# Kernel optimization log

Measured on AMD Instinct MI355X. Metric: run time of the kernel, lower is better.

## Reference

```python
import jax, jax.numpy as jnp
import numpy as np

N_TAGS = 64
SOS, EOS, PAD = 61, 62, 63
NEG = -1000000.0
B, S = 512, 1024


def setup_inputs() -> dict:
    key = jax.random.key(0)
    k1, k2, k3 = jax.random.split(key, 3)
    emissions = jax.random.normal(k1, (B, S, N_TAGS), dtype=jnp.float32)
    tags = jax.random.randint(k2, (B, S), 0, SOS)  # real tags only
    mask = jnp.ones((B, S), dtype=jnp.float32)
    t = jax.random.uniform(k3, (N_TAGS, N_TAGS), minval=-0.1, maxval=0.1, dtype=jnp.float32)
    t = t.at[:, SOS].set(NEG)
    t = t.at[EOS, :].set(NEG)
    t = t.at[PAD, :].set(NEG)
    t = t.at[:, PAD].set(NEG)
    t = t.at[PAD, EOS].set(0.0)
    t = t.at[PAD, PAD].set(0.0)
    return {"emissions": emissions, "tags": tags, "mask": mask, "transitions": t}


def _crf_nll(emissions, tags, mask, transitions):
    b, s, _ = emissions.shape
    # ---- gold path score (vectorized over seq) ----
    first_tags = tags[:, 0]
    last_idx = mask.astype(jnp.int32).sum(1) - 1  # [B]
    last_tags = tags[jnp.arange(b), last_idx]
    e_all = jnp.take_along_axis(emissions, tags[..., None], axis=-1)[..., 0]  # [B,S]
    t_all = transitions[tags[:, :-1], tags[:, 1:]]  # [B,S-1]
    m_tail = mask[:, 1:]
    scores = (
        transitions[SOS, first_tags]
        + e_all[:, 0]
        + jnp.sum((e_all[:, 1:] + t_all) * m_tail, axis=1)
        + transitions[last_tags, EOS]
    )
    # ---- log partition: sequential logsumexp scan ----
    alphas0 = transitions[SOS][None, :] + emissions[:, 0]  # [B,T]

    def step(alphas, inp):
        em_i, m_i = inp  # [B,T], [B]
        # scores[b, prev, cur] = alphas[b,prev] + transitions[prev,cur] + em[b,cur]
        sc = alphas[:, :, None] + transitions[None, :, :] + em_i[:, None, :]
        new_alphas = jax.nn.logsumexp(sc, axis=1)  # [B,T]
        alphas = m_i[:, None] * new_alphas + (1.0 - m_i[:, None]) * alphas
        return alphas, None

    xs = (jnp.swapaxes(emissions[:, 1:], 0, 1), jnp.swapaxes(mask[:, 1:], 0, 1))
    alphas, _ = jax.lax.scan(step, alphas0, xs)
    log_z = jax.nn.logsumexp(alphas + transitions[:, EOS][None, :], axis=1)  # [B]
    return -jnp.sum(scores - log_z)


def reference(emissions, tags, mask, transitions):
    return _crf_nll(emissions, tags, mask, transitions)
```

## Files before the change

### kernel.cpp

```cpp
#include <hip/hip_runtime.h>

#define NTAG 64
#define SOS_T 61
#define EOS_T 62
#define BB 512
#define SS 1024
#define LOG2E 1.4426950408889634f
#define LN2   0.6931471805599453f

#define STEP(EF, MK, RESC) do {                                              \
    float q0_=0.f,q1_=0.f,q2_=0.f,q3_=0.f,q4_=0.f,q5_=0.f,q6_=0.f,q7_=0.f;   \
    unsigned mxu_ = 0u;                                                      \
    _Pragma("unroll")                                                        \
    for (int i_ = 0; i_ < 64; ++i_) {                                        \
        unsigned ab_ = (unsigned)__builtin_amdgcn_readlane(                  \
                            (int)__float_as_uint(A), i_);                    \
        float av_ = __uint_as_float(ab_);                                    \
        switch (i_ & 7) {                                                    \
            case 0: q0_ = fmaf(av_, eT[i_], q0_); break;                     \
            case 1: q1_ = fmaf(av_, eT[i_], q1_); break;                     \
            case 2: q2_ = fmaf(av_, eT[i_], q2_); break;                     \
            case 3: q3_ = fmaf(av_, eT[i_], q3_); break;                     \
            case 4: q4_ = fmaf(av_, eT[i_], q4_); break;                     \
            case 5: q5_ = fmaf(av_, eT[i_], q5_); break;                     \
            case 6: q6_ = fmaf(av_, eT[i_], q6_); break;                     \
            default: q7_ = fmaf(av_, eT[i_], q7_); break;                    \
        }                                                                    \
        if (RESC) mxu_ = (ab_ > mxu_) ? ab_ : mxu_;                          \
    }                                                                        \
    float qq_ = ((q0_+q1_)+(q2_+q3_)) + ((q4_+q5_)+(q6_+q7_));               \
    float An_ = qq_ * (EF);                                                  \
    A = ((MK) != 0.f) ? An_ : A;                                             \
    if (RESC) {                                                              \
        int e_ = (int)(mxu_ >> 23) - 127;                                    \
        e_ = (mxu_ == 0u) ? 0 : e_;                                          \
        float sc_ = __uint_as_float((unsigned)(127 - e_) << 23);             \
        A *= sc_;                                                            \
        Mint += e_;                                                          \
    }                                                                        \
} while (0)

__global__ __launch_bounds__(64) void crf_nll_kernel(
    const float* __restrict__ emissions,
    const int*   __restrict__ tags,
    const float* __restrict__ mask,
    const float* __restrict__ trans,
    float* __restrict__ out)
{
    const int b = blockIdx.x;
    const int j = threadIdx.x;

    __shared__ __align__(16) float T_lds[NTAG * NTAG];
    __shared__ __align__(16) float mask_lds[SS];

    const float4* tg4 = (const float4*)trans;
    float4* tl4 = (float4*)T_lds;
#pragma unroll
    for (int i = 0; i < 16; ++i) tl4[i * 64 + j] = tg4[i * 64 + j];

    float eT[NTAG];
#pragma unroll
    for (int i = 0; i < NTAG; ++i)
        eT[i] = exp2f(trans[i * NTAG + j] * LOG2E);
    __syncthreads();

    const float* emb_g = emissions + (size_t)b * SS * NTAG;
    const int*   tgb   = tags + (size_t)b * SS;
    const float* mkb   = mask + (size_t)b * SS;

    float sc = 0.f, ms = 0.f;
#pragma unroll 4
    for (int k = 0; k < SS / 64; ++k) {
        int t = k * 64 + j;
        int tg = tgb[t];
        float m = mkb[t];
        mask_lds[t] = m;
        ms += m;
        float e = emb_g[t * NTAG + tg];
        if (t == 0) {
            sc += T_lds[SOS_T * NTAG + tg] + e;
        } else {
            int tgp = tgb[t - 1];
            sc += m * (e + T_lds[tgp * NTAG + tg]);
        }
    }
#pragma unroll
    for (int o = 32; o > 0; o >>= 1) {
        sc += __shfl_xor(sc, o);
        ms += __shfl_xor(ms, o);
    }
    int last_idx = (int)(ms + 0.5f) - 1;
    int last_tag = tgb[last_idx];
    sc += T_lds[last_tag * NTAG + EOS_T];

    float A = exp2f((T_lds[SOS_T * NTAG + j] + emb_g[j]) * LOG2E);
    int Mint = 0;

    float er[16];
#pragma unroll
    for (int k = 0; k < 16; ++k) er[k] = emb_g[(1 + k) * NTAG + j];

#pragma unroll 1
    for (int tb = 1; tb <= SS - 31; tb += 16) {
        float ef[16];
#pragma unroll
        for (int k = 0; k < 16; ++k) ef[k] = exp2f(er[k] * LOG2E);
#pragma unroll
        for (int k = 0; k < 16; ++k) {
            int tn = tb + 16 + k;
            tn = (tn > SS - 1) ? (SS - 1) : tn;
            er[k] = emb_g[tn * NTAG + j];
        }
        float mk[16];
#pragma unroll
        for (int k = 0; k < 16; ++k) mk[k] = mask_lds[tb + k];

        STEP(ef[0],  mk[0],  false);
        STEP(ef[1],  mk[1],  false);
        STEP(ef[2],  mk[2],  false);
        STEP(ef[3],  mk[3],  false);
        STEP(ef[4],  mk[4],  false);
        STEP(ef[5],  mk[5],  false);
        STEP(ef[6],  mk[6],  false);
        STEP(ef[7],  mk[7],  true);
        STEP(ef[8],  mk[8],  false);
        STEP(ef[9],  mk[9],  false);
        STEP(ef[10], mk[10], false);
        STEP(ef[11], mk[11], false);
        STEP(ef[12], mk[12], false);
        STEP(ef[13], mk[13], false);
        STEP(ef[14], mk[14], false);
        STEP(ef[15], mk[15], true);
    }
    {
        float ef[15];
#pragma unroll
        for (int k = 0; k < 15; ++k) ef[k] = exp2f(er[k] * LOG2E);
        float mk[15];
#pragma unroll
        for (int k = 0; k < 15; ++k) mk[k] = mask_lds[SS - 15 + k];

        STEP(ef[0],  mk[0],  false);
        STEP(ef[1],  mk[1],  false);
        STEP(ef[2],  mk[2],  false);
        STEP(ef[3],  mk[3],  false);
        STEP(ef[4],  mk[4],  false);
        STEP(ef[5],  mk[5],  false);
        STEP(ef[6],  mk[6],  false);
        STEP(ef[7],  mk[7],  true);
        STEP(ef[8],  mk[8],  false);
        STEP(ef[9],  mk[9],  false);
        STEP(ef[10], mk[10], false);
        STEP(ef[11], mk[11], false);
        STEP(ef[12], mk[12], false);
        STEP(ef[13], mk[13], false);
        STEP(ef[14], mk[14], false);
    }

    float val = A * exp2f(T_lds[j * NTAG + EOS_T] * LOG2E);
#pragma unroll
    for (int o = 32; o > 0; o >>= 1) val += __shfl_xor(val, o);
    float log_z = (log2f(val) + (float)Mint) * LN2;

    if (j == 0) atomicAdd(out, log_z - sc);
}

extern "C" void kernel_launch(void* const* d_in, const int* in_sizes, int n_in,
                              void* d_out, int out_size, void* d_ws, size_t ws_size,
                              hipStream_t stream) {
    const float* emissions = (const float*)d_in[0];
    const int*   tags      = (const int*)d_in[1];
    const float* mask      = (const float*)d_in[2];
    const float* trans     = (const float*)d_in[3];
    float* out = (float*)d_out;

    hipMemsetAsync(out, 0, sizeof(float), stream);
    crf_nll_kernel<<<dim3(BB), dim3(64), 0, stream>>>(emissions, tags, mask, trans, out);
}
```

Measured before the change: 264.0 us.

## Use packed FMA with bpermute broadcast and per-step DPP max rescaling

Replaces the 64 scalar readlane broadcasts per step with ds_bpermute pairs feeding v_pk_fma_f32, which halves the FMA instruction count by processing two previous-tag terms at once. Rescaling now happens every step: a DPP max-reduction computes the exponent, which is applied lagged by one step via a multiply folded into the emission factor. The aim is to cut the SALU/readlane serialization in the recurrence, at the cost of LDS-path bpermute latency and extra DPP instructions on every step.

```diff
diff --git a/kernel.cpp b/kernel.cpp
--- a/kernel.cpp
+++ b/kernel.cpp
@@ -8,36 +8,46 @@
 #define LOG2E 1.4426950408889634f
 #define LN2   0.6931471805599453f
 
-#define STEP(EF, MK, RESC) do {                                              \
-    float q0_=0.f,q1_=0.f,q2_=0.f,q3_=0.f,q4_=0.f,q5_=0.f,q6_=0.f,q7_=0.f;   \
-    unsigned mxu_ = 0u;                                                      \
+typedef float v2f __attribute__((ext_vector_type(2)));
+
+template<int CTRL>
+__device__ __forceinline__ float dppfmax(float x) {
+    int xi = __float_as_int(x);
+    int yi = __builtin_amdgcn_update_dpp(xi, xi, CTRL, 0xf, 0xf, false);
+    return fmaxf(x, __int_as_float(yi));
+}
+
+#define STEP(EF, MK) do {                                                    \
+    int Ai_ = __float_as_int(A);                                             \
+    v2f q0_ = {0.f, 0.f}, q1_ = q0_, q2_ = q0_, q3_ = q0_;                   \
     _Pragma("unroll")                                                        \
-    for (int i_ = 0; i_ < 64; ++i_) {                                        \
-        unsigned ab_ = (unsigned)__builtin_amdgcn_readlane(                  \
-                            (int)__float_as_uint(A), i_);                    \
-        float av_ = __uint_as_float(ab_);                                    \
-        switch (i_ & 7) {                                                    \
-            case 0: q0_ = fmaf(av_, eT[i_], q0_); break;                     \
-            case 1: q1_ = fmaf(av_, eT[i_], q1_); break;                     \
-            case 2: q2_ = fmaf(av_, eT[i_], q2_); break;                     \
-            case 3: q3_ = fmaf(av_, eT[i_], q3_); break;                     \
-            case 4: q4_ = fmaf(av_, eT[i_], q4_); break;                     \
-            case 5: q5_ = fmaf(av_, eT[i_], q5_); break;                     \
-            case 6: q6_ = fmaf(av_, eT[i_], q6_); break;                     \
-            default: q7_ = fmaf(av_, eT[i_], q7_); break;                    \
+    for (int s_ = 0; s_ < 32; ++s_) {                                        \
+        int bl_ = __builtin_amdgcn_ds_bpermute(8 * s_,     Ai_);             \
+        int bh_ = __builtin_amdgcn_ds_bpermute(8 * s_ + 4, Ai_);             \
+        v2f av_;                                                             \
+        av_.x = __int_as_float(bl_);                                         \
+        av_.y = __int_as_float(bh_);                                         \
+        switch (s_ & 3) {                                                    \
+            case 0: asm("v_pk_fma_f32 %0, %1, %2, %0" : "+v"(q0_) : "v"(av_), "v"(eT2[s_])); break; \
+            case 1: asm("v_pk_fma_f32 %0, %1, %2, %0" : "+v"(q1_) : "v"(av_), "v"(eT2[s_])); break; \
+            case 2: asm("v_pk_fma_f32 %0, %1, %2, %0" : "+v"(q2_) : "v"(av_), "v"(eT2[s_])); break; \
+            default: asm("v_pk_fma_f32 %0, %1, %2, %0" : "+v"(q3_) : "v"(av_), "v"(eT2[s_])); break; \
         }                                                                    \
-        if (RESC) mxu_ = (ab_ > mxu_) ? ab_ : mxu_;                          \
     }                                                                        \
-    float qq_ = ((q0_+q1_)+(q2_+q3_)) + ((q4_+q5_)+(q6_+q7_));               \
-    float An_ = qq_ * (EF);                                                  \
+    v2f qs_ = (q0_ + q1_) + (q2_ + q3_);                                     \
+    float qq_ = qs_.x + qs_.y;                                               \
+    float An_ = qq_ * ((EF) * sc1);                                          \
     A = ((MK) != 0.f) ? An_ : A;                                             \
-    if (RESC) {                                                              \
-        int e_ = (int)(mxu_ >> 23) - 127;                                    \
-        e_ = (mxu_ == 0u) ? 0 : e_;                                          \
-        float sc_ = __uint_as_float((unsigned)(127 - e_) << 23);             \
-        A *= sc_;                                                            \
-        Mint += e_;                                                          \
-    }                                                                        \
+    Mf = fmaf((MK), e1, Mf);                                                 \
+    float mx_ = dppfmax<0xB1>(A);             \
+    mx_ = dppfmax<0x4E>(mx_);                 \
+    mx_ = dppfmax<0x141>(mx_);                \
+    mx_ = dppfmax<0x140>(mx_);                \
+    mx_ = dppfmax<0x142>(mx_);                \
+    mx_ = dppfmax<0x143>(mx_);           \
+    int me_ = (__builtin_amdgcn_readlane(__float_as_int(mx_), 63) >> 23) - 127; \
+    sc1 = __int_as_float((127 - me_) << 23);                                 \
+    e1  = (float)me_;                                                        \
 } while (0)
 
 __global__ __launch_bounds__(64) void crf_nll_kernel(
@@ -58,10 +68,12 @@
 #pragma unroll
     for (int i = 0; i < 16; ++i) tl4[i * 64 + j] = tg4[i * 64 + j];
 
-    float eT[NTAG];
+    v2f eT2[32];
 #pragma unroll
-    for (int i = 0; i < NTAG; ++i)
-        eT[i] = exp2f(trans[i * NTAG + j] * LOG2E);
+    for (int i = 0; i < 32; ++i) {
+        eT2[i].x = exp2f(trans[(2 * i + 0) * NTAG + j] * LOG2E);
+        eT2[i].y = exp2f(trans[(2 * i + 1) * NTAG + j] * LOG2E);
+    }
     __syncthreads();
 
     const float* emb_g = emissions + (size_t)b * SS * NTAG;
@@ -94,7 +106,9 @@
     sc += T_lds[last_tag * NTAG + EOS_T];
 
     float A = exp2f((T_lds[SOS_T * NTAG + j] + emb_g[j]) * LOG2E);
-    int Mint = 0;
+    float Mf = 0.f;
+    float sc1 = 1.0f;
+    float e1  = 0.0f;
 
     float er[16];
 #pragma unroll
@@ -115,22 +129,22 @@
 #pragma unroll
         for (int k = 0; k < 16; ++k) mk[k] = mask_lds[tb + k];
 
-        STEP(ef[0],  mk[0],  false);
-        STEP(ef[1],  mk[1],  false);
-        STEP(ef[2],  mk[2],  false);
-        STEP(ef[3],  mk[3],  false);
-        STEP(ef[4],  mk[4],  false);
-        STEP(ef[5],  mk[5],  false);
-        STEP(ef[6],  mk[6],  false);
-        STEP(ef[7],  mk[7],  true);
-        STEP(ef[8],  mk[8],  false);
-        STEP(ef[9],  mk[9],  false);
-        STEP(ef[10], mk[10], false);
-        STEP(ef[11], mk[11], false);
-        STEP(ef[12], mk[12], false);
-        STEP(ef[13], mk[13], false);
-        STEP(ef[14], mk[14], false);
-        STEP(ef[15], mk[15], true);
+        STEP(ef[0],  mk[0]);
+        STEP(ef[1],  mk[1]);
+        STEP(ef[2],  mk[2]);
+        STEP(ef[3],  mk[3]);
+        STEP(ef[4],  mk[4]);
+        STEP(ef[5],  mk[5]);
+        STEP(ef[6],  mk[6]);
+        STEP(ef[7],  mk[7]);
+        STEP(ef[8],  mk[8]);
+        STEP(ef[9],  mk[9]);
+        STEP(ef[10], mk[10]);
+        STEP(ef[11], mk[11]);
+        STEP(ef[12], mk[12]);
+        STEP(ef[13], mk[13]);
+        STEP(ef[14], mk[14]);
+        STEP(ef[15], mk[15]);
     }
     {
         float ef[15];
@@ -140,27 +154,27 @@
 #pragma unroll
         for (int k = 0; k < 15; ++k) mk[k] = mask_lds[SS - 15 + k];
 
-        STEP(ef[0],  mk[0],  false);
-        STEP(ef[1],  mk[1],  false);
-        STEP(ef[2],  mk[2],  false);
-        STEP(ef[3],  mk[3],  false);
-        STEP(ef[4],  mk[4],  false);
-        STEP(ef[5],  mk[5],  false);
-        STEP(ef[6],  mk[6],  false);
-        STEP(ef[7],  mk[7],  true);
-        STEP(ef[8],  mk[8],  false);
-        STEP(ef[9],  mk[9],  false);
-        STEP(ef[10], mk[10], false);
-        STEP(ef[11], mk[11], false);
-        STEP(ef[12], mk[12], false);
-        STEP(ef[13], mk[13], false);
-        STEP(ef[14], mk[14], false);
+        STEP(ef[0],  mk[0]);
+        STEP(ef[1],  mk[1]);
+        STEP(ef[2],  mk[2]);
+        STEP(ef[3],  mk[3]);
+        STEP(ef[4],  mk[4]);
+        STEP(ef[5],  mk[5]);
+        STEP(ef[6],  mk[6]);
+        STEP(ef[7],  mk[7]);
+        STEP(ef[8],  mk[8]);
+        STEP(ef[9],  mk[9]);
+        STEP(ef[10], mk[10]);
+        STEP(ef[11], mk[11]);
+        STEP(ef[12], mk[12]);
+        STEP(ef[13], mk[13]);
+        STEP(ef[14], mk[14]);
     }
 
     float val = A * exp2f(T_lds[j * NTAG + EOS_T] * LOG2E);
 #pragma unroll
     for (int o = 32; o > 0; o >>= 1) val += __shfl_xor(val, o);
-    float log_z = (log2f(val) + (float)Mint) * LN2;
+    float log_z = (log2f(val) + Mf) * LN2;
 
     if (j == 0) atomicAdd(out, log_z - sc);
 }
```

After: 430.4 us. 1.63x slower.
